# Performance work log

Hardware: AMD Instinct MI355X
Metric: run time of the kernel (lower is better)

## Reference

```python
import jax, jax.numpy as jnp
import numpy as np

N, E, ORDER, D, RANK = 4096, 16384, 3, 13, 128
NUM_PARAMS = ORDER + 1  # BT mode: ids = edge_types[:, i] in [0, order+1)
NUM_ITERS = 3
ATOMS = 7


def setup_inputs() -> dict:
    key = jax.random.key(0)
    ks = jax.random.split(key, 9)
    nodes = jax.random.normal(ks[0], (N, D), dtype=jnp.float32)
    edges = jax.random.randint(ks[1], (E, ORDER), 0, N)
    edge_types = jax.random.randint(ks[2], (E, ORDER), 0, NUM_PARAMS)
    atoms = jax.random.randint(ks[3], (E,), 0, ATOMS)
    atom_edges = jax.random.randint(ks[4], (E, ORDER), 0, ATOMS)
    # BPNet.params / bias: uniform(-1/sqrt(rank), 1/sqrt(rank))
    s1 = 1.0 / np.sqrt(RANK).astype(np.float32)
    bp_params = jax.random.uniform(ks[5], (NUM_PARAMS, D, RANK), minval=-s1, maxval=s1, dtype=jnp.float32)
    bp_bias = jax.random.uniform(ks[6], (NUM_PARAMS, 1, RANK), minval=-s1, maxval=s1, dtype=jnp.float32)
    # HighorderNet params per slot i: [NUM_PARAMS, hidden=RANK, out=D], uniform(-1/sqrt(D), 1/sqrt(D))
    s2 = 1.0 / np.sqrt(D).astype(np.float32)
    ho_params = jax.random.uniform(ks[7], (ORDER, NUM_PARAMS, RANK, D), minval=-s2, maxval=s2, dtype=jnp.float32)
    ho_bias = jax.random.uniform(ks[8], (ORDER, NUM_PARAMS, 1, D), minval=-s2, maxval=s2, dtype=jnp.float32)
    return {"nodes": nodes, "bp_params": bp_params, "bp_bias": bp_bias,
            "ho_params": ho_params, "ho_bias": ho_bias,
            "edges": edges, "edge_types": edge_types, "atoms": atoms, "atom_edges": atom_edges}


def _forward(nodes, bp_params, bp_bias, ho_params, ho_bias, edges, edge_types):
    n_nodes = nodes.shape[0]
    order = edges.shape[1]
    # Stage 1: per-slot gathered matmul rnodes @ W[edge_type] + b, then relu.
    rn = nodes[edges]                        # [E, order, D]
    W = bp_params[edge_types]                # [E, order, D, RANK]
    b = bp_bias[edge_types][:, :, 0, :]      # [E, order, RANK]
    t = jax.nn.relu(jnp.einsum('eod,eodr->eor', rn, W) + b)
    t = jnp.transpose(t, (1, 0, 2))          # [order, E, RANK]
    # Iterated message passing. NOTE: original loop re-reads the same
    # transform_cat each iteration (it is never updated), so every iteration
    # recomputes identical node_msg; we keep the loop for structural fidelity.
    node_msg = jnp.zeros((n_nodes, nodes.shape[1]), nodes.dtype)
    for _ in range(NUM_ITERS):
        node_msg = jnp.zeros((n_nodes, nodes.shape[1]), nodes.dtype)
        for i in range(order):
            # leave-one-out product over the other slots -> [E, RANK]
            others = [t[j] for j in range(order) if j != i]
            fact = others[0]
            for o in others[1:]:
                fact = fact * o
            Wi = ho_params[i][edge_types[:, i]]      # [E, RANK, D]
            bi = ho_bias[i][edge_types[:, i], 0]     # [E, D]
            msg = jnp.einsum('er,erd->ed', fact, Wi) + bi
            # dense one-hot incidence matmul == scatter-add over target nodes
            node_msg = node_msg + jax.ops.segment_sum(msg, edges[:, i], num_segments=n_nodes)
    return node_msg


def reference(nodes, bp_params, bp_bias, ho_params, ho_bias, edges, edge_types, atoms, atom_edges):
    # atoms / atom_edges unused in 'BT' mode (kept for signature fidelity)
    return _forward(nodes, bp_params, bp_bias, ho_params, ho_bias, edges, edge_types)
```

## Files before the change

kernel.cpp:

```cpp
#include <hip/hip_runtime.h>


#define DD 13
#define OD 3
#define NP 4
#define RK 128

typedef unsigned int uint;

#define W2P_OFF 0
#define W2P_N   (12 * 13 * 68)
#define W1P_OFF (W2P_OFF + W2P_N)
#define W1P_N   (4 * 13 * 68)
#define B1Q_OFF (W1P_OFF + W1P_N)
#define B1Q_N   (4 * 68)
#define HOB_OFF (B1Q_OFF + B1Q_N)
#define HOB_N   (12 * 16)
#define TAB_N   (HOB_OFF + HOB_N)
#define NROW_N  (4 * 24 * 16)
#define SH_N    (TAB_N + NROW_N)

__device__ __forceinline__ uint bf16pair(float lo, float hi) {
    uint ul = __float_as_uint(lo);
    uint uh = __float_as_uint(hi);
    ul += 0x7fffu + ((ul >> 16) & 1u);
    uh += 0x7fffu + ((uh >> 16) & 1u);
    return (ul >> 16) | (uh & 0xffff0000u);
}
__device__ __forceinline__ float bflo(uint w) { return __uint_as_float(w << 16); }
__device__ __forceinline__ float bfhi(uint w) { return __uint_as_float(w & 0xffff0000u); }

template <int CTRL>
__device__ __forceinline__ float dpp_add(float x) {
    int p = __builtin_amdgcn_update_dpp(0, __float_as_int(x), CTRL, 0xF, 0xF, false);
    return x + __int_as_float(p);
}
__device__ __forceinline__ float row_sum16(float x) {
    x = dpp_add<0xB1>(x);
    x = dpp_add<0x4E>(x);
    x = dpp_add<0x141>(x);
    x = dpp_add<0x140>(x);
    return x;
}

__global__ __launch_bounds__(256) void bpnet_pack(
    const float* __restrict__ bp_params,
    const float* __restrict__ bp_bias,
    const float* __restrict__ ho_params,
    const float* __restrict__ ho_bias,
    uint* __restrict__ ws)
{
    const int tid = blockIdx.x * 256 + threadIdx.x;
    if (tid < W1P_OFF) {
        const int c = tid % 68, q = tid / 68;
        const int dd = q % 13, it = q / 13;
        uint v = 0;
        if (c < 64)
            v = bf16pair(ho_params[(size_t)(it * RK + 2 * c) * DD + dd],
                         ho_params[(size_t)(it * RK + 2 * c + 1) * DD + dd]);
        ws[tid] = v;
    } else if (tid < B1Q_OFF) {
        const int j = tid - W1P_OFF;
        const int c = j % 68, q = j / 68;
        const int d = q % 13, ty = q / 13;
        uint v = 0;
        if (c < 64)
            v = bf16pair(bp_params[(ty * DD + d) * RK + 2 * c],
                         bp_params[(ty * DD + d) * RK + 2 * c + 1]);
        ws[tid] = v;
    } else if (tid < HOB_OFF) {
        const int j = tid - B1Q_OFF;
        const int c = j % 68, ty = j / 68;
        uint v = 0;
        if (c < 64)
            v = bf16pair(bp_bias[ty * RK + 2 * c], bp_bias[ty * RK + 2 * c + 1]);
        ws[tid] = v;
    } else if (tid < TAB_N) {
        const int j = tid - HOB_OFF;
        const int dd = j % 16, it = j / 16;
        ((float*)ws)[tid] = (dd < DD) ? ho_bias[it * DD + dd] : 0.f;
    }
}

__global__ __launch_bounds__(256, 2) void bpnet_fused(
    const float* __restrict__ nodes,
    const int*   __restrict__ edges,
    const int*   __restrict__ edge_types,
    const uint*  __restrict__ tab,
    float*       __restrict__ out)
{
    __shared__ __align__(16) uint sh[SH_N];
    const int tid = threadIdx.x;

    for (int k4 = tid; k4 < TAB_N / 4; k4 += 256)
        ((uint4*)sh)[k4] = ((const uint4*)tab)[k4];
    __syncthreads();

    const uint*  w2p = sh + W2P_OFF;
    const uint*  w1p = sh + W1P_OFF;
    const uint*  b1q = sh + B1Q_OFF;
    const float* hob = (const float*)(sh + HOB_OFF);
    float* nrow = (float*)(sh + TAB_N);

    const int lane = tid & 63;
    const int wv   = tid >> 6;
    const int e4   = lane >> 4;
    const int g    = lane & 15;
    const int eb   = (blockIdx.x * 4 + wv) * 8;

    int ev = 0, tv = 0;
    if (lane < 24) {
        ev = edges[eb * OD + lane];
        tv = edge_types[eb * OD + lane];
    }
    float* mynr = nrow + wv * (24 * 16);
#pragma unroll
    for (int c = 0; c < 5; ++c) {
        const int idx = c * 64 + lane;
        if (idx < 312) {
            const int r = idx / 13, col = idx - r * 13;
            const int nr_ = __shfl(ev, r, 64);
            mynr[r * 16 + col] = nodes[(size_t)nr_ * DD + col];
        }
    }

#pragma unroll 1
    for (int ch = 0; ch < 2; ++ch) {
        int tg[OD], et[OD];
#pragma unroll
        for (int i = 0; i < OD; ++i) {
            tg[i] = __shfl(ev, ch * 12 + e4 * 3 + i, 64);
            et[i] = __shfl(tv, ch * 12 + e4 * 3 + i, 64);
        }

        float t[OD][8];
#pragma unroll
        for (int o = 0; o < OD; ++o) {
            const float* nr_ = mynr + (ch * 12 + e4 * 3 + o) * 16;
            const float4 nA = *(const float4*)(nr_);
            const float4 nB = *(const float4*)(nr_ + 4);
            const float4 nC = *(const float4*)(nr_ + 8);
            const float  nD = nr_[12];
            const uint* wq = w1p + (et[o] * 13) * 68 + 4 * g;
            const uint4 bq = *(const uint4*)(b1q + et[o] * 68 + 4 * g);
            float s[8] = {bflo(bq.x), bfhi(bq.x), bflo(bq.y), bfhi(bq.y),
                          bflo(bq.z), bfhi(bq.z), bflo(bq.w), bfhi(bq.w)};
#define S1(dn, nv_) { const uint4 w = *(const uint4*)(wq + (dn) * 68);       \
            s[0] = fmaf(nv_, bflo(w.x), s[0]); s[1] = fmaf(nv_, bfhi(w.x), s[1]); \
            s[2] = fmaf(nv_, bflo(w.y), s[2]); s[3] = fmaf(nv_, bfhi(w.y), s[3]); \
            s[4] = fmaf(nv_, bflo(w.z), s[4]); s[5] = fmaf(nv_, bfhi(w.z), s[5]); \
            s[6] = fmaf(nv_, bflo(w.w), s[6]); s[7] = fmaf(nv_, bfhi(w.w), s[7]); }
            S1(0, nA.x) S1(1, nA.y) S1(2, nA.z) S1(3, nA.w)
            S1(4, nB.x) S1(5, nB.y) S1(6, nB.z) S1(7, nB.w)
            S1(8, nC.x) S1(9, nC.y) S1(10, nC.z) S1(11, nC.w)
            S1(12, nD)
#undef S1
#pragma unroll
            for (int r = 0; r < 8; ++r) t[o][r] = fmaxf(s[r], 0.f);
        }

#pragma unroll
        for (int i = 0; i < OD; ++i) {
            const int j = (i + 1) % OD, k = (i + 2) % OD;
            float f[8];
#pragma unroll
            for (int r = 0; r < 8; ++r) f[r] = t[j][r] * t[k][r];
            const int it = i * NP + et[i];
            const uint* wq2 = w2p + (it * 13) * 68 + 4 * g;
            float c[DD];
#pragma unroll
            for (int dd = 0; dd < DD; ++dd) {
                const uint4 w = *(const uint4*)(wq2 + dd * 68);
                float a = f[0] * bflo(w.x);
                a = fmaf(f[1], bfhi(w.x), a);
                a = fmaf(f[2], bflo(w.y), a);
                a = fmaf(f[3], bfhi(w.y), a);
                a = fmaf(f[4], bflo(w.z), a);
                a = fmaf(f[5], bfhi(w.z), a);
                a = fmaf(f[6], bflo(w.w), a);
                a = fmaf(f[7], bfhi(w.w), a);
                c[dd] = a;
            }
#pragma unroll
            for (int dd = 0; dd < DD; ++dd) c[dd] = row_sum16(c[dd]);
            float q = c[0];
#pragma unroll
            for (int dd = 1; dd < DD; ++dd) q = (g == dd) ? c[dd] : q;
            q += hob[it * 16 + g];
            if (g < DD) atomicAdd(out + (size_t)tg[i] * DD + g, q);
        }
    }
}

extern "C" void kernel_launch(void* const* d_in, const int* in_sizes, int n_in,
                              void* d_out, int out_size, void* d_ws, size_t ws_size,
                              hipStream_t stream) {
    const float* nodes      = (const float*)d_in[0];
    const float* bp_params  = (const float*)d_in[1];
    const float* bp_bias    = (const float*)d_in[2];
    const float* ho_params  = (const float*)d_in[3];
    const float* ho_bias    = (const float*)d_in[4];
    const int*   edges      = (const int*)d_in[5];
    const int*   edge_types = (const int*)d_in[6];
    float* out = (float*)d_out;
    uint*  ws  = (uint*)d_ws;

    const int E = in_sizes[5] / OD;

    hipMemsetAsync(out, 0, (size_t)out_size * sizeof(float), stream);

    bpnet_pack<<<(TAB_N + 255) / 256, 256, 0, stream>>>(
        bp_params, bp_bias, ho_params, ho_bias, ws);

    bpnet_fused<<<E / 32, 256, 0, stream>>>(
        nodes, edges, edge_types, ws, out);
}
```

Measured before the change: 87.85 us.

## Switch weights to fp16 with packed dot2 and reshape blocks to 512 threads

Replaces the bf16-packed weights and scalar FMA chains with fp16 pairs consumed by v_dot2 instructions for both the stage-1 transform and the output projection. Node rows are also packed to fp16 pairs. Each block now has 8 waves handling 4 edges each instead of 4 waves handling 8 edges over two chunks. The padded 68-stride layouts are dropped. This halves the arithmetic instruction count and LDS traffic per edge, at the cost of fp16 range and precision limits on activations and products, and a different occupancy and LDS footprint.

```diff
diff --git a/kernel.cpp b/kernel.cpp
--- a/kernel.cpp
+++ b/kernel.cpp
@@ -7,28 +7,25 @@
 #define RK 128
 
 typedef unsigned int uint;
+typedef _Float16 h2 __attribute__((ext_vector_type(2)));
 
-#define W2P_OFF 0
-#define W2P_N   (12 * 13 * 68)
-#define W1P_OFF (W2P_OFF + W2P_N)
-#define W1P_N   (4 * 13 * 68)
-#define B1Q_OFF (W1P_OFF + W1P_N)
-#define B1Q_N   (4 * 68)
-#define HOB_OFF (B1Q_OFF + B1Q_N)
+#define W2H_OFF 0
+#define W2H_N   (12 * 13 * 64)
+#define W1H_OFF (W2H_OFF + W2H_N)
+#define W1H_N   (4 * 7 * 128)
+#define B1F_OFF (W1H_OFF + W1H_N)
+#define B1F_N   (4 * 128)
+#define HOB_OFF (B1F_OFF + B1F_N)
 #define HOB_N   (12 * 16)
 #define TAB_N   (HOB_OFF + HOB_N)
-#define NROW_N  (4 * 24 * 16)
+#define NROW_OFF TAB_N
+#define NROW_N  (8 * 12 * 8)
 #define SH_N    (TAB_N + NROW_N)
 
-__device__ __forceinline__ uint bf16pair(float lo, float hi) {
-    uint ul = __float_as_uint(lo);
-    uint uh = __float_as_uint(hi);
-    ul += 0x7fffu + ((ul >> 16) & 1u);
-    uh += 0x7fffu + ((uh >> 16) & 1u);
-    return (ul >> 16) | (uh & 0xffff0000u);
+__device__ __forceinline__ uint pk(float lo, float hi) {
+    return __builtin_bit_cast(uint, __builtin_amdgcn_cvt_pkrtz(lo, hi));
 }
-__device__ __forceinline__ float bflo(uint w) { return __uint_as_float(w << 16); }
-__device__ __forceinline__ float bfhi(uint w) { return __uint_as_float(w & 0xffff0000u); }
+__device__ __forceinline__ h2 ash2(uint w) { return __builtin_bit_cast(h2, w); }
 
 template <int CTRL>
 __device__ __forceinline__ float dpp_add(float x) {
@@ -51,38 +48,28 @@
     uint* __restrict__ ws)
 {
     const int tid = blockIdx.x * 256 + threadIdx.x;
-    if (tid < W1P_OFF) {
-        const int c = tid % 68, q = tid / 68;
+    if (tid < W1H_OFF) {
+        const int c = tid & 63, q = tid >> 6;
         const int dd = q % 13, it = q / 13;
-        uint v = 0;
-        if (c < 64)
-            v = bf16pair(ho_params[(size_t)(it * RK + 2 * c) * DD + dd],
-                         ho_params[(size_t)(it * RK + 2 * c + 1) * DD + dd]);
-        ws[tid] = v;
-    } else if (tid < B1Q_OFF) {
-        const int j = tid - W1P_OFF;
-        const int c = j % 68, q = j / 68;
-        const int d = q % 13, ty = q / 13;
-        uint v = 0;
-        if (c < 64)
-            v = bf16pair(bp_params[(ty * DD + d) * RK + 2 * c],
-                         bp_params[(ty * DD + d) * RK + 2 * c + 1]);
-        ws[tid] = v;
+        ws[tid] = pk(ho_params[(size_t)(it * RK + 2 * c) * DD + dd],
+                     ho_params[(size_t)(it * RK + 2 * c + 1) * DD + dd]);
+    } else if (tid < B1F_OFF) {
+        const int j = tid - W1H_OFF;
+        const int r = j & 127, q = j >> 7;
+        const int p = q % 7, ty = q / 7;
+        const float a = bp_params[(ty * DD + 2 * p) * RK + r];
+        const float b = (2 * p + 1 < DD) ? bp_params[(ty * DD + 2 * p + 1) * RK + r] : 0.f;
+        ws[tid] = pk(a, b);
     } else if (tid < HOB_OFF) {
-        const int j = tid - B1Q_OFF;
-        const int c = j % 68, ty = j / 68;
-        uint v = 0;
-        if (c < 64)
-            v = bf16pair(bp_bias[ty * RK + 2 * c], bp_bias[ty * RK + 2 * c + 1]);
-        ws[tid] = v;
+        ((float*)ws)[tid] = bp_bias[tid - B1F_OFF];
     } else if (tid < TAB_N) {
         const int j = tid - HOB_OFF;
-        const int dd = j % 16, it = j / 16;
+        const int dd = j & 15, it = j >> 4;
         ((float*)ws)[tid] = (dd < DD) ? ho_bias[it * DD + dd] : 0.f;
     }
 }
 
-__global__ __launch_bounds__(256, 2) void bpnet_fused(
+__global__ __launch_bounds__(512, 4) void bpnet_fused(
     const float* __restrict__ nodes,
     const int*   __restrict__ edges,
     const int*   __restrict__ edge_types,
@@ -92,103 +79,99 @@
     __shared__ __align__(16) uint sh[SH_N];
     const int tid = threadIdx.x;
 
-    for (int k4 = tid; k4 < TAB_N / 4; k4 += 256)
+    for (int k4 = tid; k4 < TAB_N / 4; k4 += 512)
         ((uint4*)sh)[k4] = ((const uint4*)tab)[k4];
     __syncthreads();
-
-    const uint*  w2p = sh + W2P_OFF;
-    const uint*  w1p = sh + W1P_OFF;
-    const uint*  b1q = sh + B1Q_OFF;
-    const float* hob = (const float*)(sh + HOB_OFF);
-    float* nrow = (float*)(sh + TAB_N);
 
     const int lane = tid & 63;
     const int wv   = tid >> 6;
     const int e4   = lane >> 4;
     const int g    = lane & 15;
-    const int eb   = (blockIdx.x * 4 + wv) * 8;
+    const int eb   = (blockIdx.x * 8 + wv) * 4;
 
     int ev = 0, tv = 0;
-    if (lane < 24) {
+    if (lane < 12) {
         ev = edges[eb * OD + lane];
         tv = edge_types[eb * OD + lane];
     }
-    float* mynr = nrow + wv * (24 * 16);
+
+    uint* mynr = sh + NROW_OFF + wv * 96;
 #pragma unroll
-    for (int c = 0; c < 5; ++c) {
-        const int idx = c * 64 + lane;
-        if (idx < 312) {
-            const int r = idx / 13, col = idx - r * 13;
+    for (int pass = 0; pass < 2; ++pass) {
+        const int idx = pass * 64 + lane;
+        if (idx < 96) {
+            const int r = idx >> 3, p = idx & 7;
             const int nr_ = __shfl(ev, r, 64);
-            mynr[r * 16 + col] = nodes[(size_t)nr_ * DD + col];
+            uint v = 0;
+            if (p < 6)       v = pk(nodes[(size_t)nr_ * DD + 2 * p],
+                                    nodes[(size_t)nr_ * DD + 2 * p + 1]);
+            else if (p == 6) v = pk(nodes[(size_t)nr_ * DD + 12], 0.f);
+            mynr[r * 8 + p] = v;
         }
     }
 
-#pragma unroll 1
-    for (int ch = 0; ch < 2; ++ch) {
-        int tg[OD], et[OD];
+    int tg[OD], et[OD];
 #pragma unroll
-        for (int i = 0; i < OD; ++i) {
-            tg[i] = __shfl(ev, ch * 12 + e4 * 3 + i, 64);
-            et[i] = __shfl(tv, ch * 12 + e4 * 3 + i, 64);
-        }
+    for (int i = 0; i < OD; ++i) {
+        tg[i] = __shfl(ev, e4 * OD + i, 64);
+        et[i] = __shfl(tv, e4 * OD + i, 64);
+    }
 
-        float t[OD][8];
+    float t[OD][8];
 #pragma unroll
-        for (int o = 0; o < OD; ++o) {
-            const float* nr_ = mynr + (ch * 12 + e4 * 3 + o) * 16;
-            const float4 nA = *(const float4*)(nr_);
-            const float4 nB = *(const float4*)(nr_ + 4);
-            const float4 nC = *(const float4*)(nr_ + 8);
-            const float  nD = nr_[12];
-            const uint* wq = w1p + (et[o] * 13) * 68 + 4 * g;
-            const uint4 bq = *(const uint4*)(b1q + et[o] * 68 + 4 * g);
-            float s[8] = {bflo(bq.x), bfhi(bq.x), bflo(bq.y), bfhi(bq.y),
-                          bflo(bq.z), bfhi(bq.z), bflo(bq.w), bfhi(bq.w)};
-#define S1(dn, nv_) { const uint4 w = *(const uint4*)(wq + (dn) * 68);       \
-            s[0] = fmaf(nv_, bflo(w.x), s[0]); s[1] = fmaf(nv_, bfhi(w.x), s[1]); \
-            s[2] = fmaf(nv_, bflo(w.y), s[2]); s[3] = fmaf(nv_, bfhi(w.y), s[3]); \
-            s[4] = fmaf(nv_, bflo(w.z), s[4]); s[5] = fmaf(nv_, bfhi(w.z), s[5]); \
-            s[6] = fmaf(nv_, bflo(w.w), s[6]); s[7] = fmaf(nv_, bfhi(w.w), s[7]); }
-            S1(0, nA.x) S1(1, nA.y) S1(2, nA.z) S1(3, nA.w)
-            S1(4, nB.x) S1(5, nB.y) S1(6, nB.z) S1(7, nB.w)
-            S1(8, nC.x) S1(9, nC.y) S1(10, nC.z) S1(11, nC.w)
-            S1(12, nD)
+    for (int o = 0; o < OD; ++o) {
+        const uint* nh = mynr + (e4 * OD + o) * 8;
+        const uint4 n0 = *(const uint4*)(nh);
+        const uint4 n1 = *(const uint4*)(nh + 4);
+        const float* bf = (const float*)(sh + B1F_OFF) + et[o] * RK + 8 * g;
+        const float4 b0 = *(const float4*)(bf);
+        const float4 b1 = *(const float4*)(bf + 4);
+        float s[8] = {b0.x, b0.y, b0.z, b0.w, b1.x, b1.y, b1.z, b1.w};
+        const uint* wb = sh + W1H_OFF + (et[o] * 7) * RK + 8 * g;
+#define S1(p, nv) { const uint4 wA = *(const uint4*)(wb + (p) * RK);          \
+                    const uint4 wB = *(const uint4*)(wb + (p) * RK + 4);      \
+            const h2 nn = ash2(nv);                                           \
+            s[0] = __builtin_amdgcn_fdot2(nn, ash2(wA.x), s[0], false);       \
+            s[1] = __builtin_amdgcn_fdot2(nn, ash2(wA.y), s[1], false);       \
+            s[2] = __builtin_amdgcn_fdot2(nn, ash2(wA.z), s[2], false);       \
+            s[3] = __builtin_amdgcn_fdot2(nn, ash2(wA.w), s[3], false);       \
+            s[4] = __builtin_amdgcn_fdot2(nn, ash2(wB.x), s[4], false);       \
+            s[5] = __builtin_amdgcn_fdot2(nn, ash2(wB.y), s[5], false);       \
+            s[6] = __builtin_amdgcn_fdot2(nn, ash2(wB.z), s[6], false);       \
+            s[7] = __builtin_amdgcn_fdot2(nn, ash2(wB.w), s[7], false); }
+        S1(0, n0.x) S1(1, n0.y) S1(2, n0.z) S1(3, n0.w)
+        S1(4, n1.x) S1(5, n1.y) S1(6, n1.z)
 #undef S1
 #pragma unroll
-            for (int r = 0; r < 8; ++r) t[o][r] = fmaxf(s[r], 0.f);
-        }
+        for (int r = 0; r < 8; ++r) t[o][r] = fmaxf(s[r], 0.f);
+    }
 
 #pragma unroll
-        for (int i = 0; i < OD; ++i) {
-            const int j = (i + 1) % OD, k = (i + 2) % OD;
-            float f[8];
+    for (int i = 0; i < OD; ++i) {
+        const int j = (i + 1) % OD, k = (i + 2) % OD;
+        uint fh[4];
 #pragma unroll
-            for (int r = 0; r < 8; ++r) f[r] = t[j][r] * t[k][r];
-            const int it = i * NP + et[i];
-            const uint* wq2 = w2p + (it * 13) * 68 + 4 * g;
-            float c[DD];
+        for (int r = 0; r < 4; ++r)
+            fh[r] = pk(t[j][2 * r] * t[k][2 * r], t[j][2 * r + 1] * t[k][2 * r + 1]);
+        const int it = i * NP + et[i];
+        const uint* wb = sh + W2H_OFF + (it * DD) * 64 + 4 * g;
+        float c[DD];
 #pragma unroll
-            for (int dd = 0; dd < DD; ++dd) {
-                const uint4 w = *(const uint4*)(wq2 + dd * 68);
-                float a = f[0] * bflo(w.x);
-                a = fmaf(f[1], bfhi(w.x), a);
-                a = fmaf(f[2], bflo(w.y), a);
-                a = fmaf(f[3], bfhi(w.y), a);
-                a = fmaf(f[4], bflo(w.z), a);
-                a = fmaf(f[5], bfhi(w.z), a);
-                a = fmaf(f[6], bflo(w.w), a);
-                a = fmaf(f[7], bfhi(w.w), a);
-                c[dd] = a;
-            }
+        for (int dd = 0; dd < DD; ++dd) {
+            const uint4 w = *(const uint4*)(wb + dd * 64);
+            float a = __builtin_amdgcn_fdot2(ash2(fh[0]), ash2(w.x), 0.f, false);
+            a = __builtin_amdgcn_fdot2(ash2(fh[1]), ash2(w.y), a, false);
+            a = __builtin_amdgcn_fdot2(ash2(fh[2]), ash2(w.z), a, false);
+            a = __builtin_amdgcn_fdot2(ash2(fh[3]), ash2(w.w), a, false);
+            c[dd] = a;
+        }
 #pragma unroll
-            for (int dd = 0; dd < DD; ++dd) c[dd] = row_sum16(c[dd]);
-            float q = c[0];
+        for (int dd = 0; dd < DD; ++dd) c[dd] = row_sum16(c[dd]);
+        float q = c[0];
 #pragma unroll
-            for (int dd = 1; dd < DD; ++dd) q = (g == dd) ? c[dd] : q;
-            q += hob[it * 16 + g];
-            if (g < DD) atomicAdd(out + (size_t)tg[i] * DD + g, q);
-        }
+        for (int dd = 1; dd < DD; ++dd) q = (g == dd) ? c[dd] : q;
+        q += ((const float*)(sh + HOB_OFF))[it * 16 + g];
+        if (g < DD) atomicAdd(out + (size_t)tg[i] * DD + g, q);
     }
 }
 
@@ -207,11 +190,10 @@
 
     const int E = in_sizes[5] / OD;
 
-    hipMemsetAsync(out, 0, (size_t)out_size * sizeof(float), stream);
+    (void)hipMemsetAsync(out, 0, (size_t)out_size * sizeof(float), stream);
 
     bpnet_pack<<<(TAB_N + 255) / 256, 256, 0, stream>>>(
         bp_params, bp_bias, ho_params, ho_bias, ws);
 
-    bpnet_fused<<<E / 32, 256, 0, stream>>>(
-        nodes, edges, edge_types, ws, out);
+    bpnet_fused<<<E / 32, 512, 0, stream>>>(nodes, edges, edge_types, ws, out);
 }
```

New measurement: 82.87 us. 5.7% less time.
